# Optimization experiments

Hardware: AMD Instinct MI355X
Metric: run time of the kernel (lower is better)

The kernel has to match this reference:

```python
import jax, jax.numpy as jnp
import numpy as np

SOFTENING = 0.01
SOFTENING_SQ = SOFTENING * SOFTENING


def setup_inputs() -> dict:
    key = jax.random.key(0)
    k1, k2 = jax.random.split(key)
    N = 8192
    positions = jax.random.normal(k1, (N, 3), dtype=jnp.float32)
    masses = jax.random.uniform(k2, (N,), dtype=jnp.float32)
    return {"positions": positions, "masses": masses}


def reference(positions, masses):
    # diff[i, j] = r_j - r_i  -> shape (N, N, 3)
    diff = positions[None, :, :] - positions[:, None, :]
    dist_sq = jnp.sum(diff * diff, axis=2) + SOFTENING_SQ        # (N, N)
    inv_dist_cubed = dist_sq ** (-1.5)                            # (N, N)
    # a_i = sum_j m_j * diff[i, j] * inv_dist_cubed[i, j]
    w = masses[None, :] * inv_dist_cubed                          # (N, N)
    accelerations = jnp.einsum('ij,ijd->id', w, diff)             # (N, 3)
    return accelerations
```

## Files before the change

### kernel.cpp

```cpp
#include <hip/hip_runtime.h>

#define NBODY 8192
#define BLOCK 256
#define SLABS 32
#define JCHUNK (NBODY / SLABS)
#define SOFT2 1.0e-4f

__global__ __launch_bounds__(BLOCK) void nbody_kernel(
    const float* __restrict__ pos, const float* __restrict__ mass,
    float* __restrict__ out) {
  __shared__ float4 tile[JCHUNK];

  const int t = threadIdx.x;
  const int i = blockIdx.x * BLOCK + t;
  const int j0 = blockIdx.y * JCHUNK;

  const int j = j0 + t;
  tile[t] = make_float4(pos[j * 3 + 0], pos[j * 3 + 1], pos[j * 3 + 2],
                        mass[j]);

  const float xi = pos[i * 3 + 0];
  const float yi = pos[i * 3 + 1];
  const float zi = pos[i * 3 + 2];

  __syncthreads();

  float ax = 0.f, ay = 0.f, az = 0.f;
#pragma unroll 8
  for (int k = 0; k < JCHUNK; ++k) {
    float4 o = tile[k];
    float dx = o.x - xi;
    float dy = o.y - yi;
    float dz = o.z - zi;
    float r2 = fmaf(dx, dx, fmaf(dy, dy, fmaf(dz, dz, SOFT2)));
    float inv = __builtin_amdgcn_rsqf(r2);
    float w = o.w * (inv * inv * inv);
    ax = fmaf(w, dx, ax);
    ay = fmaf(w, dy, ay);
    az = fmaf(w, dz, az);
  }

  atomicAdd(&out[i * 3 + 0], ax);
  atomicAdd(&out[i * 3 + 1], ay);
  atomicAdd(&out[i * 3 + 2], az);
}

extern "C" void kernel_launch(void* const* d_in, const int* in_sizes, int n_in,
                              void* d_out, int out_size, void* d_ws,
                              size_t ws_size, hipStream_t stream) {
  const float* pos = (const float*)d_in[0];
  const float* mass = (const float*)d_in[1];
  float* out = (float*)d_out;

  hipMemsetAsync(d_out, 0, (size_t)out_size * sizeof(float), stream);

  dim3 grid(NBODY / BLOCK, SLABS);
  nbody_kernel<<<grid, BLOCK, 0, stream>>>(pos, mass, out);
}
```

Measured before the change: 78.99 us.

## Split each body's j-loop across a 32-lane group and reduce with shuffles

```diff
diff --git a/kernel.cpp b/kernel.cpp
--- a/kernel.cpp
+++ b/kernel.cpp
@@ -1,48 +1,64 @@
 #include <hip/hip_runtime.h>
 
-#define NBODY 8192
+#define N 8192
 #define BLOCK 256
-#define SLABS 32
-#define JCHUNK (NBODY / SLABS)
+#define IPB 8
+#define CHUNK 2048
 #define SOFT2 1.0e-4f
 
 __global__ __launch_bounds__(BLOCK) void nbody_kernel(
     const float* __restrict__ pos, const float* __restrict__ mass,
     float* __restrict__ out) {
-  __shared__ float4 tile[JCHUNK];
+  __shared__ float4 tile[CHUNK];
 
   const int t = threadIdx.x;
-  const int i = blockIdx.x * BLOCK + t;
-  const int j0 = blockIdx.y * JCHUNK;
-
-  const int j = j0 + t;
-  tile[t] = make_float4(pos[j * 3 + 0], pos[j * 3 + 1], pos[j * 3 + 2],
-                        mass[j]);
+  const int jl = t & 31;
+  const int il = t >> 5;
+  const int i = blockIdx.x * IPB + il;
 
   const float xi = pos[i * 3 + 0];
   const float yi = pos[i * 3 + 1];
   const float zi = pos[i * 3 + 2];
 
-  __syncthreads();
+  float ax = 0.f, ay = 0.f, az = 0.f;
 
-  float ax = 0.f, ay = 0.f, az = 0.f;
+  for (int c0 = 0; c0 < N; c0 += CHUNK) {
+    __syncthreads();
+    for (int s = t; s < CHUNK; s += BLOCK) {
+      const int j = c0 + s;
+      tile[s] = make_float4(pos[j * 3 + 0], pos[j * 3 + 1], pos[j * 3 + 2],
+                            mass[j]);
+    }
+    __syncthreads();
+
 #pragma unroll 8
-  for (int k = 0; k < JCHUNK; ++k) {
-    float4 o = tile[k];
-    float dx = o.x - xi;
-    float dy = o.y - yi;
-    float dz = o.z - zi;
-    float r2 = fmaf(dx, dx, fmaf(dy, dy, fmaf(dz, dz, SOFT2)));
-    float inv = __builtin_amdgcn_rsqf(r2);
-    float w = o.w * (inv * inv * inv);
-    ax = fmaf(w, dx, ax);
-    ay = fmaf(w, dy, ay);
-    az = fmaf(w, dz, az);
+    for (int k = jl; k < CHUNK; k += 32) {
+      float4 o = tile[k];
+      float dx = o.x - xi;
+      float dy = o.y - yi;
+      float dz = o.z - zi;
+      float r2 = fmaf(dx, dx, fmaf(dy, dy, fmaf(dz, dz, SOFT2)));
+      float inv = __builtin_amdgcn_rsqf(r2);
+      float inv2 = inv * inv;
+      float w = o.w * (inv2 * inv);
+      ax = fmaf(w, dx, ax);
+      ay = fmaf(w, dy, ay);
+      az = fmaf(w, dz, az);
+    }
   }
 
-  atomicAdd(&out[i * 3 + 0], ax);
-  atomicAdd(&out[i * 3 + 1], ay);
-  atomicAdd(&out[i * 3 + 2], az);
+#pragma unroll
+  for (int off = 16; off > 0; off >>= 1) {
+    ax += __shfl_down(ax, off, 32);
+    ay += __shfl_down(ay, off, 32);
+    az += __shfl_down(az, off, 32);
+  }
+
+  if (jl == 0) {
+    out[i * 3 + 0] = ax;
+    out[i * 3 + 1] = ay;
+    out[i * 3 + 2] = az;
+  }
 }
 
 extern "C" void kernel_launch(void* const* d_in, const int* in_sizes, int n_in,
@@ -51,9 +67,5 @@
   const float* pos = (const float*)d_in[0];
   const float* mass = (const float*)d_in[1];
   float* out = (float*)d_out;
-
-  hipMemsetAsync(d_out, 0, (size_t)out_size * sizeof(float), stream);
-
-  dim3 grid(NBODY / BLOCK, SLABS);
-  nbody_kernel<<<grid, BLOCK, 0, stream>>>(pos, mass, out);
+  nbody_kernel<<<dim3(N / IPB), BLOCK, 0, stream>>>(pos, mass, out);
 }
```

New measurement: 81.44 us. 1.03x slower.

## Exploit pairwise force symmetry to halve interaction computations

Applied to the files above, without the earlier changes.

```diff
diff --git a/kernel.cpp b/kernel.cpp
--- a/kernel.cpp
+++ b/kernel.cpp
@@ -1,48 +1,84 @@
 #include <hip/hip_runtime.h>
 
-#define NBODY 8192
-#define BLOCK 256
-#define SLABS 32
-#define JCHUNK (NBODY / SLABS)
+#define N 8192
+#define TILE 64
+#define T (N / TILE)
 #define SOFT2 1.0e-4f
 
-__global__ __launch_bounds__(BLOCK) void nbody_kernel(
+__global__ __launch_bounds__(TILE) void nbody_sym(
     const float* __restrict__ pos, const float* __restrict__ mass,
     float* __restrict__ out) {
-  __shared__ float4 tile[JCHUNK];
+  const int TI = blockIdx.x;
+  const int q = blockIdx.y;
+  const int TJ = (TI + q) & (T - 1);
+  if (q == T / 2 && TI >= T / 2) return;
 
-  const int t = threadIdx.x;
-  const int i = blockIdx.x * BLOCK + t;
-  const int j0 = blockIdx.y * JCHUNK;
+  __shared__ float4 jb[TILE];
+  __shared__ float4 jacc[TILE];
 
-  const int j = j0 + t;
-  tile[t] = make_float4(pos[j * 3 + 0], pos[j * 3 + 1], pos[j * 3 + 2],
-                        mass[j]);
+  const int l = threadIdx.x;
+  const int i = TI * TILE + l;
+  const int j = TJ * TILE + l;
+
+  jb[l] = make_float4(pos[j * 3 + 0], pos[j * 3 + 1], pos[j * 3 + 2], mass[j]);
+  jacc[l] = make_float4(0.f, 0.f, 0.f, 0.f);
 
   const float xi = pos[i * 3 + 0];
   const float yi = pos[i * 3 + 1];
   const float zi = pos[i * 3 + 2];
+  const float mi = mass[i];
 
+  float ax = 0.f, ay = 0.f, az = 0.f;
   __syncthreads();
 
-  float ax = 0.f, ay = 0.f, az = 0.f;
+  if (q == 0) {
 #pragma unroll 8
-  for (int k = 0; k < JCHUNK; ++k) {
-    float4 o = tile[k];
-    float dx = o.x - xi;
-    float dy = o.y - yi;
-    float dz = o.z - zi;
-    float r2 = fmaf(dx, dx, fmaf(dy, dy, fmaf(dz, dz, SOFT2)));
-    float inv = __builtin_amdgcn_rsqf(r2);
-    float w = o.w * (inv * inv * inv);
-    ax = fmaf(w, dx, ax);
-    ay = fmaf(w, dy, ay);
-    az = fmaf(w, dz, az);
+    for (int k = 0; k < TILE; ++k) {
+      float4 o = jb[k];
+      float dx = o.x - xi;
+      float dy = o.y - yi;
+      float dz = o.z - zi;
+      float r2 = fmaf(dx, dx, fmaf(dy, dy, fmaf(dz, dz, SOFT2)));
+      float inv = __builtin_amdgcn_rsqf(r2);
+      float w = o.w * (inv * inv * inv);
+      ax = fmaf(w, dx, ax);
+      ay = fmaf(w, dy, ay);
+      az = fmaf(w, dz, az);
+    }
+    atomicAdd(&out[i * 3 + 0], ax);
+    atomicAdd(&out[i * 3 + 1], ay);
+    atomicAdd(&out[i * 3 + 2], az);
+  } else {
+#pragma unroll 8
+    for (int k = 0; k < TILE; ++k) {
+      const int jj = (l + k) & (TILE - 1);
+      float4 o = jb[jj];
+      float dx = o.x - xi;
+      float dy = o.y - yi;
+      float dz = o.z - zi;
+      float r2 = fmaf(dx, dx, fmaf(dy, dy, fmaf(dz, dz, SOFT2)));
+      float inv = __builtin_amdgcn_rsqf(r2);
+      float inv3 = inv * inv * inv;
+      float wj = o.w * inv3;
+      float wi = mi * inv3;
+      ax = fmaf(wj, dx, ax);
+      ay = fmaf(wj, dy, ay);
+      az = fmaf(wj, dz, az);
+      float4 acc = jacc[jj];
+      acc.x = fmaf(-wi, dx, acc.x);
+      acc.y = fmaf(-wi, dy, acc.y);
+      acc.z = fmaf(-wi, dz, acc.z);
+      jacc[jj] = acc;
+    }
+    atomicAdd(&out[i * 3 + 0], ax);
+    atomicAdd(&out[i * 3 + 1], ay);
+    atomicAdd(&out[i * 3 + 2], az);
+    __syncthreads();
+    float4 ja = jacc[l];
+    atomicAdd(&out[j * 3 + 0], ja.x);
+    atomicAdd(&out[j * 3 + 1], ja.y);
+    atomicAdd(&out[j * 3 + 2], ja.z);
   }
-
-  atomicAdd(&out[i * 3 + 0], ax);
-  atomicAdd(&out[i * 3 + 1], ay);
-  atomicAdd(&out[i * 3 + 2], az);
 }
 
 extern "C" void kernel_launch(void* const* d_in, const int* in_sizes, int n_in,
@@ -54,6 +90,5 @@
 
   hipMemsetAsync(d_out, 0, (size_t)out_size * sizeof(float), stream);
 
-  dim3 grid(NBODY / BLOCK, SLABS);
-  nbody_kernel<<<grid, BLOCK, 0, stream>>>(pos, mass, out);
+  nbody_sym<<<dim3(T, T / 2 + 1), TILE, 0, stream>>>(pos, mass, out);
 }
```

New measurement: 92.79 us. 1.17x slower.
